# Performance work log

Measured on AMD Instinct MI355X. Metric: run time of the kernel, lower is better.

Reference implementation:

```python
import jax, jax.numpy as jnp
import numpy as np

N_NODES = 100000
N_EDGES = 1600000
D = 64


def setup_inputs() -> dict:
    key = jax.random.key(0)
    k1, k2, k3 = jax.random.split(key, 3)
    x = jax.random.normal(k1, (N_NODES, D), dtype=jnp.float32)
    edge_index = jax.random.randint(k2, (2, N_EDGES), 0, N_NODES, dtype=jnp.int32)
    W = jax.random.normal(k3, (D, D), dtype=jnp.float32) * 0.05  # linear weight [out_dim, in_dim]
    b = jnp.zeros((D,), dtype=jnp.float32)
    return {"x": x, "edge_index": edge_index, "W": W, "b": b}


def reference(x, edge_index, W, b):
    n = x.shape[0]
    # add self loops
    loops = jnp.arange(n, dtype=edge_index.dtype)
    src = jnp.concatenate([edge_index[0], loops])
    dst = jnp.concatenate([edge_index[1], loops])
    # in-degree (counting self loops) via scatter-add of ones onto dst
    deg = jax.ops.segment_sum(jnp.ones_like(src, dtype=x.dtype), dst, num_segments=n)
    deg_inv_sqrt = jnp.where(deg > 0, jax.lax.rsqrt(jnp.maximum(deg, 1.0)) * (deg > 0), 0.0)
    deg_inv_sqrt = jnp.where(deg > 0, deg ** -0.5, 0.0)
    # per-edge symmetric normalization, gather-scale-scatter
    norm = deg_inv_sqrt[src] * deg_inv_sqrt[dst]  # [E+N]
    msgs = x[src] * norm[:, None]                  # [E+N, D] big irregular gather
    out = jax.ops.segment_sum(msgs, dst, num_segments=n)  # scatter-add to nodes
    # dense linear
    return out @ W.T + b
```

## Files before the change

kernel.cpp:

```cpp
#include <hip/hip_runtime.h>


#define BSHIFT 7
#define BNODES 128
#define CAP 3072
#define EPB 4096
#define SMEM_BYTES 33792

__device__ inline unsigned short f2b_rn(float f) {
    unsigned u = __float_as_uint(f);
    unsigned r = u + 0x7FFFu + ((u >> 16) & 1u);
    return (unsigned short)(r >> 16);
}
__device__ inline float b2f(unsigned short h) {
    return __uint_as_float(((unsigned)h) << 16);
}

__global__ __launch_bounds__(256) void fused_gemm_scatter_kernel(
    const float* __restrict__ x, const float* __restrict__ W, ushort4* __restrict__ yh,
    const int* __restrict__ ei, int* __restrict__ gcur, unsigned int* __restrict__ grec,
    int n, int e, int nbuck, int sblocks) {
    __shared__ __align__(16) unsigned char smem[SMEM_BYTES];
    int t = threadIdx.x;

    if ((int)blockIdx.x < sblocks) {
        unsigned int* lrec = (unsigned int*)smem;
        unsigned short* lbk = (unsigned short*)(smem + 16384);
        int* lh = (int*)(smem + 24576);
        int* lbase = lh + nbuck;
        for (int i = t; i < nbuck; i += 256) lh[i] = 0;
        __syncthreads();
        int e0 = blockIdx.x * EPB;
        int m = e - e0;
        if (m > EPB) m = EPB;
        for (int i = t; i < m; i += 256) {
            int g = e0 + i;
            int s = ei[g];
            int d = ei[e + g];
            int b = d >> BSHIFT;
            lrec[i] = ((unsigned int)s << BSHIFT) | (unsigned int)(d & (BNODES - 1));
            lbk[i] = (unsigned short)b;
            atomicAdd(&lh[b], 1);
        }
        __syncthreads();
        for (int b = t; b < nbuck; b += 256) {
            int c = lh[b];
            lbase[b] = c ? atomicAdd(&gcur[b], c) : 0;
            lh[b] = 0;
        }
        __syncthreads();
        for (int i = t; i < m; i += 256) {
            int b = lbk[i];
            int pos = lbase[b] + atomicAdd(&lh[b], 1);
            if (pos < CAP)
                grec[(size_t)b * CAP + pos] = lrec[i];
        }
    } else {
        float* At = (float*)smem;
        float* Wt = (float*)(smem + 17408);
        int m0 = ((int)blockIdx.x - sblocks) * 64;

#pragma unroll
        for (int j = 0; j < 16; ++j) {
            int idx = t + j * 256;
            int o = idx >> 6, k = idx & 63;
            Wt[k * 64 + o] = W[idx];
        }
#pragma unroll
        for (int j = 0; j < 16; ++j) {
            int idx = t + j * 256;
            int mm = idx >> 6, k = idx & 63;
            int gm = m0 + mm;
            At[k * 68 + mm] = (gm < n) ? x[(size_t)gm * 64 + k] : 0.f;
        }
        __syncthreads();

        int tx = t & 15, ty = t >> 4;
        float acc[4][4];
#pragma unroll
        for (int i = 0; i < 4; ++i)
#pragma unroll
            for (int j = 0; j < 4; ++j) acc[i][j] = 0.f;

#pragma unroll 8
        for (int k = 0; k < 64; ++k) {
            float4 a = *(const float4*)&At[k * 68 + ty * 4];
            float4 w = *(const float4*)&Wt[k * 64 + tx * 4];
            float av[4] = {a.x, a.y, a.z, a.w};
            float wv[4] = {w.x, w.y, w.z, w.w};
#pragma unroll
            for (int i = 0; i < 4; ++i)
#pragma unroll
                for (int j = 0; j < 4; ++j) acc[i][j] += av[i] * wv[j];
        }

#pragma unroll
        for (int i = 0; i < 4; ++i) {
            int gm = m0 + ty * 4 + i;
            if (gm < n) {
                ushort4 h;
                h.x = f2b_rn(acc[i][0]);
                h.y = f2b_rn(acc[i][1]);
                h.z = f2b_rn(acc[i][2]);
                h.w = f2b_rn(acc[i][3]);
                yh[(size_t)gm * 16 + tx] = h;
            }
        }
    }
}

__global__ __launch_bounds__(256) void bucket_csr_kernel(unsigned int* __restrict__ grec,
                                                         const int* __restrict__ gcur,
                                                         int* __restrict__ offb,
                                                         int* __restrict__ offe,
                                                         float* __restrict__ dis, int n) {
    __shared__ unsigned int recs[CAP];
    __shared__ int lh[BNODES];
    __shared__ int ls[BNODES];
    __shared__ int wtot;
    int t = threadIdx.x;
    int lane = t & 63;
    int b = blockIdx.x;
    size_t base = (size_t)b * CAP;
    int cnt = gcur[b];
    if (cnt > CAP) cnt = CAP;
    int node0 = b << BSHIFT;

    if (t < BNODES) lh[t] = 0;
    __syncthreads();
    for (int i = t; i < cnt; i += 256) {
        unsigned int r = grec[base + i];
        recs[i] = r;
        atomicAdd(&lh[r & (BNODES - 1)], 1);
    }
    __syncthreads();
    int c = (t < BNODES) ? lh[t] : 0;
    int v = c;
#pragma unroll
    for (int o = 1; o < 64; o <<= 1) {
        int u = __shfl_up(v, o, 64);
        if (lane >= o) v += u;
    }
    if (t == 63) wtot = v;
    __syncthreads();
    if (t >= 64 && t < BNODES) v += wtot;
    int ex = v - c;
    if (t < BNODES) {
        int node = node0 + t;
        if (node < n) {
            offb[node] = (int)base + ex;
            offe[node] = (int)base + ex + c;
            dis[node] = rsqrtf((float)(c + 1));
        }
        ls[t] = ex;
        lh[t] = 0;
    }
    __syncthreads();
    for (int i = t; i < cnt; i += 256) {
        unsigned int r = recs[i];
        int nd = r & (BNODES - 1);
        int pos = ls[nd] + atomicAdd(&lh[nd], 1);
        grec[base + pos] = r >> BSHIFT;
    }
}

__global__ __launch_bounds__(256) void gather_kernel(const ushort4* __restrict__ yh,
                                                     const unsigned int* __restrict__ srcs,
                                                     const int* __restrict__ offb,
                                                     const int* __restrict__ offe,
                                                     const float* __restrict__ dis,
                                                     const float* __restrict__ bias,
                                                     float4* __restrict__ out, int n) {
    int wid = (blockIdx.x * 256 + threadIdx.x) >> 6;
    int lane = threadIdx.x & 63;
    if (wid >= n) return;
    int grp = lane >> 4;
    int fq = lane & 15;
    int beg = offb[wid];
    int end = offe[wid];
    float dn = dis[wid];
    float4 acc = {0.f, 0.f, 0.f, 0.f};
    if (grp == 0) {
        ushort4 h = yh[(size_t)wid * 16 + fq];
        acc.x = b2f(h.x) * dn; acc.y = b2f(h.y) * dn;
        acc.z = b2f(h.z) * dn; acc.w = b2f(h.w) * dn;
    }
    for (int c = beg; c < end; c += 64) {
        int k = end - c;
        if (k > 64) k = 64;
        int sidx = 0;
        float dv = 0.f;
        if (lane < k) {
            sidx = (int)srcs[c + lane];
            dv = dis[sidx];
        }
        for (int j = 0; j < k; j += 4) {
            int jj = j + grp;
            int s = __shfl(sidx, jj);
            float w = __shfl(dv, jj);
            ushort4 h = yh[(size_t)s * 16 + fq];
            acc.x += b2f(h.x) * w;
            acc.y += b2f(h.y) * w;
            acc.z += b2f(h.z) * w;
            acc.w += b2f(h.w) * w;
        }
    }
    for (int m = 16; m < 64; m <<= 1) {
        acc.x += __shfl_xor(acc.x, m);
        acc.y += __shfl_xor(acc.y, m);
        acc.z += __shfl_xor(acc.z, m);
        acc.w += __shfl_xor(acc.w, m);
    }
    if (lane < 16) {
        float4 bb = ((const float4*)bias)[fq];
        float4 o;
        o.x = acc.x * dn + bb.x;
        o.y = acc.y * dn + bb.y;
        o.z = acc.z * dn + bb.z;
        o.w = acc.w * dn + bb.w;
        out[(size_t)wid * 16 + lane] = o;
    }
}

extern "C" void kernel_launch(void* const* d_in, const int* in_sizes, int n_in,
                              void* d_out, int out_size, void* d_ws, size_t ws_size,
                              hipStream_t stream) {
    const float* x    = (const float*)d_in[0];
    const int*   ei   = (const int*)d_in[1];
    const float* W    = (const float*)d_in[2];
    const float* bias = (const float*)d_in[3];
    float* out = (float*)d_out;

    int n = in_sizes[0] / 64;
    int e = in_sizes[1] / 2;
    int nbuck = (n + BNODES - 1) / BNODES;

    auto align = [](size_t v) { return (v + 255) & ~(size_t)255; };
    char* p = (char*)d_ws;
    int* gcur = (int*)p;          p += align((size_t)nbuck * 4);
    int* offb = (int*)p;          p += align((size_t)n * 4);
    int* offe = (int*)p;          p += align((size_t)n * 4);
    float* dis = (float*)p;       p += align((size_t)n * 4);
    unsigned int* grec = (unsigned int*)p;  p += align((size_t)nbuck * CAP * 4);
    ushort4* yh = (ushort4*)p;

    int sblocks = (e + EPB - 1) / EPB;
    int gblocks = (n + 63) / 64;

    hipMemsetAsync(gcur, 0, (size_t)nbuck * 4, stream);
    fused_gemm_scatter_kernel<<<sblocks + gblocks, 256, 0, stream>>>(
        x, W, yh, ei, gcur, grec, n, e, nbuck, sblocks);
    bucket_csr_kernel<<<nbuck, 256, 0, stream>>>(grec, gcur, offb, offe, dis, n);
    gather_kernel<<<(n + 3) / 4, 256, 0, stream>>>(yh, grec, offb, offe, dis, bias,
                                                   (float4*)out, n);
}
```

Measured before the change: 191.1 us.

## Merge all stages into one persistent cooperative kernel with grid syncs

Replaces the memset and three kernel launches with a single cooperative persistent kernel. Grid-wide syncs separate the stages: bucket scatter, dynamic-tile GEMM, per-bucket CSR build and gather. The scatter stage now reads the edge list twice instead of staging records in LDS. The GEMM tile shrinks to 32 rows and is handed out through an atomic counter. This removes launch gaps and memset overhead, at the cost of grid-sync latency and occupancy limited by the persistent grid; it also assumes 256 CUs when sizing the grid.

```diff
diff --git a/kernel.cpp b/kernel.cpp
--- a/kernel.cpp
+++ b/kernel.cpp
@@ -1,11 +1,16 @@
 #include <hip/hip_runtime.h>
+#include <hip/hip_cooperative_groups.h>
+
+namespace cg = cooperative_groups;
 
 
 #define BSHIFT 7
 #define BNODES 128
 #define CAP 3072
 #define EPB 4096
-#define SMEM_BYTES 33792
+#define GEMM_ROWS 32
+#define AT_STRIDE 34
+#define SMEM_BYTES 25088
 
 __device__ inline unsigned short f2b_rn(float f) {
     unsigned u = __float_as_uint(f);
@@ -16,209 +21,225 @@
     return __uint_as_float(((unsigned)h) << 16);
 }
 
-__global__ __launch_bounds__(256) void fused_gemm_scatter_kernel(
-    const float* __restrict__ x, const float* __restrict__ W, ushort4* __restrict__ yh,
-    const int* __restrict__ ei, int* __restrict__ gcur, unsigned int* __restrict__ grec,
-    int n, int e, int nbuck, int sblocks) {
+__global__ __launch_bounds__(256) void mega_kernel(
+    const float* __restrict__ x, const float* __restrict__ W,
+    const float* __restrict__ bias, const int* __restrict__ ei,
+    float* __restrict__ out,
+    int* __restrict__ gcur, int* __restrict__ tileCtr,
+    unsigned int* __restrict__ grec,
+    int* __restrict__ offb, int* __restrict__ offe, float* __restrict__ dis,
+    ushort4* __restrict__ yh,
+    int n, int e, int nbuck, int nchunks, int ntiles) {
     __shared__ __align__(16) unsigned char smem[SMEM_BYTES];
+    __shared__ int cur_tile;
+    __shared__ int wtot;
+    cg::grid_group grid = cg::this_grid();
     int t = threadIdx.x;
-
-    if ((int)blockIdx.x < sblocks) {
-        unsigned int* lrec = (unsigned int*)smem;
-        unsigned short* lbk = (unsigned short*)(smem + 16384);
-        int* lh = (int*)(smem + 24576);
+    int bid = blockIdx.x;
+    int G = gridDim.x;
+
+    for (int i = bid * 256 + t; i <= nbuck; i += G * 256) {
+        if (i < nbuck) gcur[i] = 0;
+        else tileCtr[0] = 0;
+    }
+    __threadfence();
+    grid.sync();
+
+    {
+        int* lh = (int*)smem;
         int* lbase = lh + nbuck;
-        for (int i = t; i < nbuck; i += 256) lh[i] = 0;
+        for (int c = bid; c < nchunks; c += G) {
+            for (int i = t; i < nbuck; i += 256) lh[i] = 0;
+            __syncthreads();
+            int e0 = c * EPB;
+            int m = e - e0;
+            if (m > EPB) m = EPB;
+            for (int i = t; i < m; i += 256)
+                atomicAdd(&lh[ei[e + e0 + i] >> BSHIFT], 1);
+            __syncthreads();
+            for (int b = t; b < nbuck; b += 256) {
+                int cc = lh[b];
+                lbase[b] = cc ? atomicAdd(&gcur[b], cc) : 0;
+                lh[b] = 0;
+            }
+            __syncthreads();
+            for (int i = t; i < m; i += 256) {
+                int g = e0 + i;
+                int s = ei[g];
+                int d = ei[e + g];
+                int b = d >> BSHIFT;
+                int pos = lbase[b] + atomicAdd(&lh[b], 1);
+                if (pos < CAP)
+                    grec[(size_t)b * CAP + pos] =
+                        ((unsigned int)s << BSHIFT) | (unsigned int)(d & (BNODES - 1));
+            }
+            __syncthreads();
+        }
+    }
+
+    {
+        float* Wt = (float*)smem;
+        float* At = (float*)(smem + 16384);
         __syncthreads();
-        int e0 = blockIdx.x * EPB;
-        int m = e - e0;
-        if (m > EPB) m = EPB;
-        for (int i = t; i < m; i += 256) {
-            int g = e0 + i;
-            int s = ei[g];
-            int d = ei[e + g];
-            int b = d >> BSHIFT;
-            lrec[i] = ((unsigned int)s << BSHIFT) | (unsigned int)(d & (BNODES - 1));
-            lbk[i] = (unsigned short)b;
-            atomicAdd(&lh[b], 1);
-        }
-        __syncthreads();
-        for (int b = t; b < nbuck; b += 256) {
-            int c = lh[b];
-            lbase[b] = c ? atomicAdd(&gcur[b], c) : 0;
-            lh[b] = 0;
-        }
-        __syncthreads();
-        for (int i = t; i < m; i += 256) {
-            int b = lbk[i];
-            int pos = lbase[b] + atomicAdd(&lh[b], 1);
-            if (pos < CAP)
-                grec[(size_t)b * CAP + pos] = lrec[i];
-        }
-    } else {
-        float* At = (float*)smem;
-        float* Wt = (float*)(smem + 17408);
-        int m0 = ((int)blockIdx.x - sblocks) * 64;
-
 #pragma unroll
         for (int j = 0; j < 16; ++j) {
             int idx = t + j * 256;
             int o = idx >> 6, k = idx & 63;
             Wt[k * 64 + o] = W[idx];
         }
-#pragma unroll
-        for (int j = 0; j < 16; ++j) {
-            int idx = t + j * 256;
-            int mm = idx >> 6, k = idx & 63;
-            int gm = m0 + mm;
-            At[k * 68 + mm] = (gm < n) ? x[(size_t)gm * 64 + k] : 0.f;
-        }
         __syncthreads();
-
-        int tx = t & 15, ty = t >> 4;
-        float acc[4][4];
-#pragma unroll
-        for (int i = 0; i < 4; ++i)
-#pragma unroll
-            for (int j = 0; j < 4; ++j) acc[i][j] = 0.f;
-
+        while (true) {
+            if (t == 0) cur_tile = atomicAdd(tileCtr, 1);
+            __syncthreads();
+            int tile = cur_tile;
+            if (tile >= ntiles) break;
+            int m0 = tile * GEMM_ROWS;
+#pragma unroll
+            for (int j = 0; j < 8; ++j) {
+                int idx = t + j * 256;
+                int mm = idx >> 6, k = idx & 63;
+                int gm = m0 + mm;
+                At[k * AT_STRIDE + mm] = (gm < n) ? x[(size_t)gm * 64 + k] : 0.f;
+            }
+            __syncthreads();
+            int tx = t & 15, ty = t >> 4;
+            float acc[2][4];
+#pragma unroll
+            for (int i = 0; i < 2; ++i)
+#pragma unroll
+                for (int j = 0; j < 4; ++j) acc[i][j] = 0.f;
 #pragma unroll 8
-        for (int k = 0; k < 64; ++k) {
-            float4 a = *(const float4*)&At[k * 68 + ty * 4];
-            float4 w = *(const float4*)&Wt[k * 64 + tx * 4];
-            float av[4] = {a.x, a.y, a.z, a.w};
-            float wv[4] = {w.x, w.y, w.z, w.w};
-#pragma unroll
-            for (int i = 0; i < 4; ++i)
-#pragma unroll
-                for (int j = 0; j < 4; ++j) acc[i][j] += av[i] * wv[j];
-        }
-
-#pragma unroll
-        for (int i = 0; i < 4; ++i) {
-            int gm = m0 + ty * 4 + i;
-            if (gm < n) {
-                ushort4 h;
-                h.x = f2b_rn(acc[i][0]);
-                h.y = f2b_rn(acc[i][1]);
-                h.z = f2b_rn(acc[i][2]);
-                h.w = f2b_rn(acc[i][3]);
-                yh[(size_t)gm * 16 + tx] = h;
-            }
-        }
-    }
-}
-
-__global__ __launch_bounds__(256) void bucket_csr_kernel(unsigned int* __restrict__ grec,
-                                                         const int* __restrict__ gcur,
-                                                         int* __restrict__ offb,
-                                                         int* __restrict__ offe,
-                                                         float* __restrict__ dis, int n) {
-    __shared__ unsigned int recs[CAP];
-    __shared__ int lh[BNODES];
-    __shared__ int ls[BNODES];
-    __shared__ int wtot;
-    int t = threadIdx.x;
-    int lane = t & 63;
-    int b = blockIdx.x;
-    size_t base = (size_t)b * CAP;
-    int cnt = gcur[b];
-    if (cnt > CAP) cnt = CAP;
-    int node0 = b << BSHIFT;
-
-    if (t < BNODES) lh[t] = 0;
-    __syncthreads();
-    for (int i = t; i < cnt; i += 256) {
-        unsigned int r = grec[base + i];
-        recs[i] = r;
-        atomicAdd(&lh[r & (BNODES - 1)], 1);
-    }
-    __syncthreads();
-    int c = (t < BNODES) ? lh[t] : 0;
-    int v = c;
-#pragma unroll
-    for (int o = 1; o < 64; o <<= 1) {
-        int u = __shfl_up(v, o, 64);
-        if (lane >= o) v += u;
-    }
-    if (t == 63) wtot = v;
-    __syncthreads();
-    if (t >= 64 && t < BNODES) v += wtot;
-    int ex = v - c;
-    if (t < BNODES) {
-        int node = node0 + t;
-        if (node < n) {
-            offb[node] = (int)base + ex;
-            offe[node] = (int)base + ex + c;
-            dis[node] = rsqrtf((float)(c + 1));
-        }
-        ls[t] = ex;
-        lh[t] = 0;
-    }
-    __syncthreads();
-    for (int i = t; i < cnt; i += 256) {
-        unsigned int r = recs[i];
-        int nd = r & (BNODES - 1);
-        int pos = ls[nd] + atomicAdd(&lh[nd], 1);
-        grec[base + pos] = r >> BSHIFT;
-    }
-}
-
-__global__ __launch_bounds__(256) void gather_kernel(const ushort4* __restrict__ yh,
-                                                     const unsigned int* __restrict__ srcs,
-                                                     const int* __restrict__ offb,
-                                                     const int* __restrict__ offe,
-                                                     const float* __restrict__ dis,
-                                                     const float* __restrict__ bias,
-                                                     float4* __restrict__ out, int n) {
-    int wid = (blockIdx.x * 256 + threadIdx.x) >> 6;
-    int lane = threadIdx.x & 63;
-    if (wid >= n) return;
-    int grp = lane >> 4;
-    int fq = lane & 15;
-    int beg = offb[wid];
-    int end = offe[wid];
-    float dn = dis[wid];
-    float4 acc = {0.f, 0.f, 0.f, 0.f};
-    if (grp == 0) {
-        ushort4 h = yh[(size_t)wid * 16 + fq];
-        acc.x = b2f(h.x) * dn; acc.y = b2f(h.y) * dn;
-        acc.z = b2f(h.z) * dn; acc.w = b2f(h.w) * dn;
-    }
-    for (int c = beg; c < end; c += 64) {
-        int k = end - c;
-        if (k > 64) k = 64;
-        int sidx = 0;
-        float dv = 0.f;
-        if (lane < k) {
-            sidx = (int)srcs[c + lane];
-            dv = dis[sidx];
-        }
-        for (int j = 0; j < k; j += 4) {
-            int jj = j + grp;
-            int s = __shfl(sidx, jj);
-            float w = __shfl(dv, jj);
-            ushort4 h = yh[(size_t)s * 16 + fq];
-            acc.x += b2f(h.x) * w;
-            acc.y += b2f(h.y) * w;
-            acc.z += b2f(h.z) * w;
-            acc.w += b2f(h.w) * w;
-        }
-    }
-    for (int m = 16; m < 64; m <<= 1) {
-        acc.x += __shfl_xor(acc.x, m);
-        acc.y += __shfl_xor(acc.y, m);
-        acc.z += __shfl_xor(acc.z, m);
-        acc.w += __shfl_xor(acc.w, m);
-    }
-    if (lane < 16) {
-        float4 bb = ((const float4*)bias)[fq];
-        float4 o;
-        o.x = acc.x * dn + bb.x;
-        o.y = acc.y * dn + bb.y;
-        o.z = acc.z * dn + bb.z;
-        o.w = acc.w * dn + bb.w;
-        out[(size_t)wid * 16 + lane] = o;
+            for (int k = 0; k < 64; ++k) {
+                float2 a = *(const float2*)&At[k * AT_STRIDE + ty * 2];
+                float4 w = *(const float4*)&Wt[k * 64 + tx * 4];
+                acc[0][0] += a.x * w.x; acc[0][1] += a.x * w.y;
+                acc[0][2] += a.x * w.z; acc[0][3] += a.x * w.w;
+                acc[1][0] += a.y * w.x; acc[1][1] += a.y * w.y;
+                acc[1][2] += a.y * w.z; acc[1][3] += a.y * w.w;
+            }
+#pragma unroll
+            for (int i = 0; i < 2; ++i) {
+                int gm = m0 + ty * 2 + i;
+                if (gm < n) {
+                    ushort4 h;
+                    h.x = f2b_rn(acc[i][0]);
+                    h.y = f2b_rn(acc[i][1]);
+                    h.z = f2b_rn(acc[i][2]);
+                    h.w = f2b_rn(acc[i][3]);
+                    yh[(size_t)gm * 16 + tx] = h;
+                }
+            }
+            __syncthreads();
+        }
+    }
+
+    __threadfence();
+    grid.sync();
+
+    {
+        unsigned int* recs = (unsigned int*)smem;
+        int* clh = (int*)(smem + 12288);
+        int* cls = (int*)(smem + 12288 + 512);
+        int lane = t & 63;
+        for (int b = bid; b < nbuck; b += G) {
+            size_t base = (size_t)b * CAP;
+            int cnt = gcur[b];
+            if (cnt > CAP) cnt = CAP;
+            int node0 = b << BSHIFT;
+            if (t < BNODES) clh[t] = 0;
+            __syncthreads();
+            for (int i = t; i < cnt; i += 256) {
+                unsigned int r = grec[base + i];
+                recs[i] = r;
+                atomicAdd(&clh[r & (BNODES - 1)], 1);
+            }
+            __syncthreads();
+            int c = (t < BNODES) ? clh[t] : 0;
+            int v = c;
+#pragma unroll
+            for (int o = 1; o < 64; o <<= 1) {
+                int u = __shfl_up(v, o, 64);
+                if (lane >= o) v += u;
+            }
+            if (t == 63) wtot = v;
+            __syncthreads();
+            if (t >= 64 && t < BNODES) v += wtot;
+            int ex = v - c;
+            if (t < BNODES) {
+                int node = node0 + t;
+                if (node < n) {
+                    offb[node] = (int)base + ex;
+                    offe[node] = (int)base + ex + c;
+                    dis[node] = rsqrtf((float)(c + 1));
+                }
+                cls[t] = ex;
+                clh[t] = 0;
+            }
+            __syncthreads();
+            for (int i = t; i < cnt; i += 256) {
+                unsigned int r = recs[i];
+                int nd = r & (BNODES - 1);
+                int pos = cls[nd] + atomicAdd(&clh[nd], 1);
+                grec[base + pos] = r >> BSHIFT;
+            }
+            __syncthreads();
+        }
+    }
+
+    __threadfence();
+    grid.sync();
+
+    {
+        int lane = t & 63;
+        int grp = lane >> 4;
+        int fq = lane & 15;
+        int gw = bid * 4 + (t >> 6);
+        for (int node = gw; node < n; node += G * 4) {
+            int beg = offb[node];
+            int end = offe[node];
+            float dn = dis[node];
+            float4 acc = {0.f, 0.f, 0.f, 0.f};
+            if (grp == 0) {
+                ushort4 h = yh[(size_t)node * 16 + fq];
+                acc.x = b2f(h.x) * dn; acc.y = b2f(h.y) * dn;
+                acc.z = b2f(h.z) * dn; acc.w = b2f(h.w) * dn;
+            }
+            for (int c = beg; c < end; c += 64) {
+                int k = end - c;
+                if (k > 64) k = 64;
+                int sidx = 0;
+                float dv = 0.f;
+                if (lane < k) {
+                    sidx = (int)grec[c + lane];
+                    dv = dis[sidx];
+                }
+                for (int j = 0; j < k; j += 4) {
+                    int jj = j + grp;
+                    int s = __shfl(sidx, jj);
+                    float w = __shfl(dv, jj);
+                    ushort4 h = yh[(size_t)s * 16 + fq];
+                    acc.x += b2f(h.x) * w;
+                    acc.y += b2f(h.y) * w;
+                    acc.z += b2f(h.z) * w;
+                    acc.w += b2f(h.w) * w;
+                }
+            }
+            for (int m = 16; m < 64; m <<= 1) {
+                acc.x += __shfl_xor(acc.x, m);
+                acc.y += __shfl_xor(acc.y, m);
+                acc.z += __shfl_xor(acc.z, m);
+                acc.w += __shfl_xor(acc.w, m);
+            }
+            if (lane < 16) {
+                float4 bb = ((const float4*)bias)[fq];
+                float4 o;
+                o.x = acc.x * dn + bb.x;
+                o.y = acc.y * dn + bb.y;
+                o.z = acc.z * dn + bb.z;
+                o.w = acc.w * dn + bb.w;
+                ((float4*)out)[(size_t)node * 16 + lane] = o;
+            }
+        }
     }
 }
 
@@ -234,23 +255,28 @@
     int n = in_sizes[0] / 64;
     int e = in_sizes[1] / 2;
     int nbuck = (n + BNODES - 1) / BNODES;
+    int nchunks = (e + EPB - 1) / EPB;
+    int ntiles = (n + GEMM_ROWS - 1) / GEMM_ROWS;
 
     auto align = [](size_t v) { return (v + 255) & ~(size_t)255; };
     char* p = (char*)d_ws;
     int* gcur = (int*)p;          p += align((size_t)nbuck * 4);
+    int* tileCtr = (int*)p;       p += align(4);
     int* offb = (int*)p;          p += align((size_t)n * 4);
     int* offe = (int*)p;          p += align((size_t)n * 4);
     float* dis = (float*)p;       p += align((size_t)n * 4);
     unsigned int* grec = (unsigned int*)p;  p += align((size_t)nbuck * CAP * 4);
     ushort4* yh = (ushort4*)p;
 
-    int sblocks = (e + EPB - 1) / EPB;
-    int gblocks = (n + 63) / 64;
-
-    hipMemsetAsync(gcur, 0, (size_t)nbuck * 4, stream);
-    fused_gemm_scatter_kernel<<<sblocks + gblocks, 256, 0, stream>>>(
-        x, W, yh, ei, gcur, grec, n, e, nbuck, sblocks);
-    bucket_csr_kernel<<<nbuck, 256, 0, stream>>>(grec, gcur, offb, offe, dis, n);
-    gather_kernel<<<(n + 3) / 4, 256, 0, stream>>>(yh, grec, offb, offe, dis, bias,
-                                                   (float4*)out, n);
-}
+    int occ = 0;
+    hipOccupancyMaxActiveBlocksPerMultiprocessor(&occ, mega_kernel, 256, 0);
+    if (occ < 1) occ = 1;
+    if (occ > 8) occ = 8;
+    int G = occ * 256;
+
+    void* args[] = {(void*)&x, (void*)&W, (void*)&bias, (void*)&ei, (void*)&out,
+                    (void*)&gcur, (void*)&tileCtr, (void*)&grec,
+                    (void*)&offb, (void*)&offe, (void*)&dis, (void*)&yh,
+                    (void*)&n, (void*)&e, (void*)&nbuck, (void*)&nchunks, (void*)&ntiles};
+    hipLaunchCooperativeKernel(mega_kernel, dim3(G), dim3(256), args, 0, stream);
+}
```

Result: slower. 584.1 us (+205.7%).

## Fuse bucket CSR build into gather kernel and prescale GEMM output by degree

Applied to the files above, without the earlier changes.

A separate histogram kernel computes in-degrees up front, so the GEMM epilogue can write Y pre-scaled by deg^-1/2. The per-edge dis[src] lookup and its shuffle disappear from the gather. The bucket sort and the gather now run in one 1024-thread kernel per bucket: edges are sorted into shared memory and each wave handles 8 nodes directly, which removes the offb/offe/dis arrays and one launch. The cost is an extra atomic histogram pass over all edges. There is also less parallelism in the gather, since each block covers only 128 nodes and work per block is imbalanced.

```diff
diff --git a/kernel.cpp b/kernel.cpp
--- a/kernel.cpp
+++ b/kernel.cpp
@@ -16,9 +16,17 @@
     return __uint_as_float(((unsigned)h) << 16);
 }
 
+__global__ __launch_bounds__(256) void hist_kernel(const int* __restrict__ dst,
+                                                   int* __restrict__ deg, int e) {
+    int i = blockIdx.x * 256 + threadIdx.x;
+    if (i < e) atomicAdd(&deg[dst[i]], 1);
+}
+
 __global__ __launch_bounds__(256) void fused_gemm_scatter_kernel(
-    const float* __restrict__ x, const float* __restrict__ W, ushort4* __restrict__ yh,
-    const int* __restrict__ ei, int* __restrict__ gcur, unsigned int* __restrict__ grec,
+    const float* __restrict__ x, const float* __restrict__ W,
+    const int* __restrict__ deg, ushort4* __restrict__ yh,
+    const int* __restrict__ ei, int* __restrict__ gcur,
+    unsigned int* __restrict__ grec,
     int n, int e, int nbuck, int sblocks) {
     __shared__ __align__(16) unsigned char smem[SMEM_BYTES];
     int t = threadIdx.x;
@@ -98,28 +106,27 @@
         for (int i = 0; i < 4; ++i) {
             int gm = m0 + ty * 4 + i;
             if (gm < n) {
+                float dn = rsqrtf((float)(deg[gm] + 1));
                 ushort4 h;
-                h.x = f2b_rn(acc[i][0]);
-                h.y = f2b_rn(acc[i][1]);
-                h.z = f2b_rn(acc[i][2]);
-                h.w = f2b_rn(acc[i][3]);
+                h.x = f2b_rn(acc[i][0] * dn);
+                h.y = f2b_rn(acc[i][1] * dn);
+                h.z = f2b_rn(acc[i][2] * dn);
+                h.w = f2b_rn(acc[i][3] * dn);
                 yh[(size_t)gm * 16 + tx] = h;
             }
         }
     }
 }
 
-__global__ __launch_bounds__(256) void bucket_csr_kernel(unsigned int* __restrict__ grec,
-                                                         const int* __restrict__ gcur,
-                                                         int* __restrict__ offb,
-                                                         int* __restrict__ offe,
-                                                         float* __restrict__ dis, int n) {
-    __shared__ unsigned int recs[CAP];
+__global__ __launch_bounds__(1024, 8) void csr_gather_kernel(
+    const unsigned int* __restrict__ grec, const int* __restrict__ gcur,
+    const ushort4* __restrict__ yh, const float* __restrict__ bias,
+    float4* __restrict__ out, int n) {
+    __shared__ unsigned int sorted[CAP];
     __shared__ int lh[BNODES];
-    __shared__ int ls[BNODES];
+    __shared__ int ls[BNODES + 1];
     __shared__ int wtot;
     int t = threadIdx.x;
-    int lane = t & 63;
     int b = blockIdx.x;
     size_t base = (size_t)b * CAP;
     int cnt = gcur[b];
@@ -128,97 +135,81 @@
 
     if (t < BNODES) lh[t] = 0;
     __syncthreads();
-    for (int i = t; i < cnt; i += 256) {
-        unsigned int r = grec[base + i];
-        recs[i] = r;
-        atomicAdd(&lh[r & (BNODES - 1)], 1);
-    }
-    __syncthreads();
-    int c = (t < BNODES) ? lh[t] : 0;
-    int v = c;
-#pragma unroll
-    for (int o = 1; o < 64; o <<= 1) {
-        int u = __shfl_up(v, o, 64);
-        if (lane >= o) v += u;
-    }
-    if (t == 63) wtot = v;
-    __syncthreads();
-    if (t >= 64 && t < BNODES) v += wtot;
-    int ex = v - c;
+    for (int i = t; i < cnt; i += 1024)
+        atomicAdd(&lh[grec[base + i] & (BNODES - 1)], 1);
+    __syncthreads();
+    int c = 0, ex = 0;
     if (t < BNODES) {
-        int node = node0 + t;
-        if (node < n) {
-            offb[node] = (int)base + ex;
-            offe[node] = (int)base + ex + c;
-            dis[node] = rsqrtf((float)(c + 1));
-        }
+        c = lh[t];
+        int lane = t & 63;
+        int v = c;
+#pragma unroll
+        for (int o = 1; o < 64; o <<= 1) {
+            int u = __shfl_up(v, o, 64);
+            if (lane >= o) v += u;
+        }
+        if (t == 63) wtot = v;
+        ex = v - c;
+    }
+    __syncthreads();
+    if (t >= 64 && t < BNODES) ex += wtot;
+    if (t < BNODES) {
         ls[t] = ex;
         lh[t] = 0;
-    }
-    __syncthreads();
-    for (int i = t; i < cnt; i += 256) {
-        unsigned int r = recs[i];
+        if (t == BNODES - 1) ls[BNODES] = ex + c;
+    }
+    __syncthreads();
+    for (int i = t; i < cnt; i += 1024) {
+        unsigned int r = grec[base + i];
         int nd = r & (BNODES - 1);
         int pos = ls[nd] + atomicAdd(&lh[nd], 1);
-        grec[base + pos] = r >> BSHIFT;
-    }
-}
-
-__global__ __launch_bounds__(256) void gather_kernel(const ushort4* __restrict__ yh,
-                                                     const unsigned int* __restrict__ srcs,
-                                                     const int* __restrict__ offb,
-                                                     const int* __restrict__ offe,
-                                                     const float* __restrict__ dis,
-                                                     const float* __restrict__ bias,
-                                                     float4* __restrict__ out, int n) {
-    int wid = (blockIdx.x * 256 + threadIdx.x) >> 6;
-    int lane = threadIdx.x & 63;
-    if (wid >= n) return;
+        sorted[pos] = r >> BSHIFT;
+    }
+    __syncthreads();
+
+    int wave = t >> 6;
+    int lane = t & 63;
     int grp = lane >> 4;
     int fq = lane & 15;
-    int beg = offb[wid];
-    int end = offe[wid];
-    float dn = dis[wid];
-    float4 acc = {0.f, 0.f, 0.f, 0.f};
-    if (grp == 0) {
-        ushort4 h = yh[(size_t)wid * 16 + fq];
-        acc.x = b2f(h.x) * dn; acc.y = b2f(h.y) * dn;
-        acc.z = b2f(h.z) * dn; acc.w = b2f(h.w) * dn;
-    }
-    for (int c = beg; c < end; c += 64) {
-        int k = end - c;
-        if (k > 64) k = 64;
-        int sidx = 0;
-        float dv = 0.f;
-        if (lane < k) {
-            sidx = (int)srcs[c + lane];
-            dv = dis[sidx];
-        }
-        for (int j = 0; j < k; j += 4) {
+    float4 bb = ((const float4*)bias)[fq];
+    for (int i = 0; i < 8; ++i) {
+        int nd = wave * 8 + i;
+        int node = node0 + nd;
+        if (node >= n) break;
+        int beg = ls[nd];
+        int end = ls[nd + 1];
+        float dn = rsqrtf((float)(end - beg) + 1.0f);
+        float4 acc = {0.f, 0.f, 0.f, 0.f};
+        if (grp == 0) {
+            ushort4 h = yh[(size_t)node * 16 + fq];
+            acc.x = b2f(h.x); acc.y = b2f(h.y);
+            acc.z = b2f(h.z); acc.w = b2f(h.w);
+        }
+        for (int j = beg; j < end; j += 4) {
             int jj = j + grp;
-            int s = __shfl(sidx, jj);
-            float w = __shfl(dv, jj);
-            ushort4 h = yh[(size_t)s * 16 + fq];
-            acc.x += b2f(h.x) * w;
-            acc.y += b2f(h.y) * w;
-            acc.z += b2f(h.z) * w;
-            acc.w += b2f(h.w) * w;
-        }
-    }
-    for (int m = 16; m < 64; m <<= 1) {
-        acc.x += __shfl_xor(acc.x, m);
-        acc.y += __shfl_xor(acc.y, m);
-        acc.z += __shfl_xor(acc.z, m);
-        acc.w += __shfl_xor(acc.w, m);
-    }
-    if (lane < 16) {
-        float4 bb = ((const float4*)bias)[fq];
-        float4 o;
-        o.x = acc.x * dn + bb.x;
-        o.y = acc.y * dn + bb.y;
-        o.z = acc.z * dn + bb.z;
-        o.w = acc.w * dn + bb.w;
-        out[(size_t)wid * 16 + lane] = o;
+            if (jj < end) {
+                int s = (int)sorted[jj];
+                ushort4 h = yh[(size_t)s * 16 + fq];
+                acc.x += b2f(h.x);
+                acc.y += b2f(h.y);
+                acc.z += b2f(h.z);
+                acc.w += b2f(h.w);
+            }
+        }
+        for (int m = 16; m < 64; m <<= 1) {
+            acc.x += __shfl_xor(acc.x, m);
+            acc.y += __shfl_xor(acc.y, m);
+            acc.z += __shfl_xor(acc.z, m);
+            acc.w += __shfl_xor(acc.w, m);
+        }
+        if (lane < 16) {
+            float4 o;
+            o.x = acc.x * dn + bb.x;
+            o.y = acc.y * dn + bb.y;
+            o.z = acc.z * dn + bb.z;
+            o.w = acc.w * dn + bb.w;
+            out[(size_t)node * 16 + lane] = o;
+        }
     }
 }
 
@@ -237,20 +228,18 @@
 
     auto align = [](size_t v) { return (v + 255) & ~(size_t)255; };
     char* p = (char*)d_ws;
+    int* deg = (int*)p;           p += align((size_t)n * 4);
     int* gcur = (int*)p;          p += align((size_t)nbuck * 4);
-    int* offb = (int*)p;          p += align((size_t)n * 4);
-    int* offe = (int*)p;          p += align((size_t)n * 4);
-    float* dis = (float*)p;       p += align((size_t)n * 4);
     unsigned int* grec = (unsigned int*)p;  p += align((size_t)nbuck * CAP * 4);
     ushort4* yh = (ushort4*)p;
 
     int sblocks = (e + EPB - 1) / EPB;
     int gblocks = (n + 63) / 64;
 
-    hipMemsetAsync(gcur, 0, (size_t)nbuck * 4, stream);
+    hipMemsetAsync(deg, 0, (size_t)((char*)(gcur + nbuck) - (char*)deg), stream);
+    hist_kernel<<<(e + 255) / 256, 256, 0, stream>>>(ei + e, deg, e);
     fused_gemm_scatter_kernel<<<sblocks + gblocks, 256, 0, stream>>>(
-        x, W, yh, ei, gcur, grec, n, e, nbuck, sblocks);
-    bucket_csr_kernel<<<nbuck, 256, 0, stream>>>(grec, gcur, offb, offe, dis, n);
-    gather_kernel<<<(n + 3) / 4, 256, 0, stream>>>(yh, grec, offb, offe, dis, bias,
-                                                   (float4*)out, n);
-}
+        x, W, deg, yh, ei, gcur, grec, n, e, nbuck, sblocks);
+    csr_gather_kernel<<<nbuck, 1024, 0, stream>>>(grec, gcur, yh, bias,
+                                                  (float4*)out, n);
+}
```

After: 242.5 us. +26.9%, slower.
